# Kernel optimization log

Hardware: AMD Instinct MI355X
Metric: run time of the kernel (lower is better)

Reference implementation:

```python
import jax, jax.numpy as jnp
import numpy as np

K = 3       # kernel_size
STRIDE = 1
PAD = 1


def conv2d(x, w, b):
    y = jax.lax.conv_general_dilated(
        x, w, window_strides=(STRIDE, STRIDE), padding=[(PAD, PAD), (PAD, PAD)],
        dimension_numbers=('NCHW', 'OIHW', 'NCHW'))
    return y + b[None, :, None, None]


def setup_inputs() -> dict:
    key = jax.random.key(0)
    ks = jax.random.split(key, 4)
    B, Cin, Cout, H, W = 8, 64, 64, 64, 64
    kk = K * K
    x = jax.random.normal(ks[0], (B, Cin, H, W), jnp.float32)
    # offset / modulator convs (zero-init in the original; use small random weights
    # so offsets are nontrivial but realistic sub-pixel scale)
    w_off = jax.random.normal(ks[1], (2 * kk, Cin, K, K), jnp.float32) * 0.01
    b_off = jnp.zeros((2 * kk,), jnp.float32)
    w_mod = jax.random.normal(ks[2], (kk, Cin, K, K), jnp.float32) * 0.01
    b_mod = jnp.zeros((kk,), jnp.float32)
    # main deformable conv weight, Kaiming-ish scale
    w = jax.random.normal(ks[3], (Cout, Cin, K, K), jnp.float32) * (1.0 / np.sqrt(Cin * kk))
    b = jnp.zeros((Cout,), jnp.float32)
    return {"x": x, "w_off": w_off, "b_off": b_off,
            "w_mod": w_mod, "b_mod": b_mod, "w": w, "b": b}


def deform_conv2d(x, offset, mask, w, b):
    # torchvision deform_conv2d semantics, deformable_groups=1, groups=1.
    B, C, H, W = x.shape
    kk = K * K
    Ho = (H + 2 * PAD - K) // STRIDE + 1
    Wo = (W + 2 * PAD - K) // STRIDE + 1
    # offset channels are interleaved (dy, dx) pairs per kernel tap
    off = offset.reshape(B, kk, 2, Ho, Wo)
    kh, kw = jnp.meshgrid(jnp.arange(K), jnp.arange(K), indexing='ij')
    kh = kh.reshape(kk).astype(x.dtype)
    kw = kw.reshape(kk).astype(x.dtype)
    base_y = (jnp.arange(Ho) * STRIDE - PAD).astype(x.dtype)
    base_x = (jnp.arange(Wo) * STRIDE - PAD).astype(x.dtype)
    # sampling coordinates in input space: [B, kk, Ho, Wo]
    ys = base_y[None, None, :, None] + kh[None, :, None, None] + off[:, :, 0]
    xs = base_x[None, None, None, :] + kw[None, :, None, None] + off[:, :, 1]
    y0 = jnp.floor(ys)
    x0 = jnp.floor(xs)

    def gather(yi, xi):
        yc = jnp.clip(yi, 0, H - 1).astype(jnp.int32)
        xc = jnp.clip(xi, 0, W - 1).astype(jnp.int32)
        # per-batch fancy gather: [C, H, W] indexed by [kk, Ho, Wo] -> [C, kk, Ho, Wo]
        return jax.vmap(lambda img, yb, xb: img[:, yb, xb])(x, yc, xc)

    acc = jnp.zeros((B, C, kk, Ho, Wo), x.dtype)
    for dy, dx in ((0, 0), (0, 1), (1, 0), (1, 1)):
        yi = y0 + dy
        xi = x0 + dx
        wgt = (1.0 - jnp.abs(ys - yi)) * (1.0 - jnp.abs(xs - xi))
        # zero-padding semantics: corners outside the input contribute 0
        valid = (yi >= 0) & (yi <= H - 1) & (xi >= 0) & (xi <= W - 1)
        wgt = jnp.where(valid, wgt, 0.0)
        acc = acc + gather(yi, xi) * wgt[:, None]
    # modulate with sigmoid mask [B, kk, Ho, Wo], then contract with conv weight
    sampled = acc * mask[:, None]
    out = jnp.einsum('bcfij,ocf->boij', sampled, w.reshape(w.shape[0], C, kk))
    return out + b[None, :, None, None]


def reference(x, w_off, b_off, w_mod, b_mod, w, b):
    offset = conv2d(x, w_off, b_off)
    mask = jax.nn.sigmoid(conv2d(x, w_mod, b_mod))
    return deform_conv2d(x, offset, mask, w, b)
```

## Files before the change

### kernel.cpp

```cpp
#include <hip/hip_runtime.h>
#include <math.h>

#define HW    64
#define NPIX  32768

typedef __attribute__((ext_vector_type(8))) short bf16x8;
typedef __attribute__((ext_vector_type(8))) short short8v;
typedef __attribute__((ext_vector_type(4))) float f32x4;

static __device__ inline short f2bf(float f) {
    union { float f; unsigned u; } v; v.f = f;
    unsigned r = v.u + 0x7fff + ((v.u >> 16) & 1);
    return (short)(r >> 16);
}
static __device__ inline float bf2f(short s) {
    union { unsigned u; float f; } v; v.u = ((unsigned)(unsigned short)s) << 16;
    return v.f;
}

__global__ void k_prep(const float* __restrict__ w,
                       const float* __restrict__ w_off,
                       const float* __restrict__ w_mod,
                       short* __restrict__ wt2, short* __restrict__ wc2) {
    int t = blockIdx.x * 256 + threadIdx.x;
    if (t < 9 * 64 * 64) {
        int c = t & 63, o = (t >> 6) & 63, f = t >> 12;
        wt2[t] = f2bf(w[(o * 64 + c) * 9 + f]);
    }
    int u = t - 9 * 64 * 64;
    if (u >= 0 && u < 9 * 32 * 64) {
        int c = u & 63, ch = (u >> 6) & 31, f = u >> 11;
        float v = 0.f;
        if (ch < 18)      v = w_off[(ch * 64 + c) * 9 + f];
        else if (ch < 27) v = w_mod[((ch - 18) * 64 + c) * 9 + f];
        wc2[u] = f2bf(v);
    }
}

__global__ __launch_bounds__(256) void k_transpose(const float* __restrict__ x,
                                                   short* __restrict__ xt) {
    __shared__ float s[64 * 65];
    int tid = threadIdx.x;
    int by  = blockIdx.x;
    int b = by >> 6, y = by & 63;
    const float* xb = x + ((size_t)b * 64) * 4096 + y * 64;
    #pragma unroll
    for (int q = 0; q < 4; ++q) {
        int fi = q * 256 + tid;
        int c = fi >> 4, xq = (fi & 15) * 4;
        float4 v = *(const float4*)(xb + (size_t)c * 4096 + xq);
        s[c * 65 + xq + 0] = v.x; s[c * 65 + xq + 1] = v.y;
        s[c * 65 + xq + 2] = v.z; s[c * 65 + xq + 3] = v.w;
    }
    __syncthreads();
    short* dst = xt + ((size_t)(b * 64 + y)) * 4096;
    #pragma unroll
    for (int q = 0; q < 4; ++q) {
        int fi = q * 256 + tid;
        int xx = fi >> 4, c = (fi & 15) * 4;
        short4 v = make_short4(f2bf(s[(c + 0) * 65 + xx]), f2bf(s[(c + 1) * 65 + xx]),
                               f2bf(s[(c + 2) * 65 + xx]), f2bf(s[(c + 3) * 65 + xx]));
        *(short4*)(dst + xx * 64 + c) = v;
    }
}

__global__ __launch_bounds__(128, 2) void k_fused(
        const short* __restrict__ xt,
        const short* __restrict__ wc2, const short* __restrict__ wt2,
        const float* __restrict__ b_off, const float* __restrict__ b_mod,
        const float* __restrict__ bias, float* __restrict__ out) {
    __shared__ __align__(16) char smem[19328];
    short*  s_in  = (short*)smem;
    float4* s_mW  = (float4*)smem;
    int4*   s_mO  = (int4*)(smem + 4608);
    float*  s_fin = (float*)smem;
    float*  s_out = (float*)(smem + 14720);

    int tid  = threadIdx.x;
    int lane = tid & 63;
    int wv   = __builtin_amdgcn_readfirstlane((int)(tid >> 6));
    int blk  = blockIdx.x;
    int b = blk >> 7, i = (blk >> 1) & 63, jb = (blk & 1) * 32;
    const short* xb = xt + (size_t)b * 262144;

    int arow = lane & 15;
    int cg   = lane >> 4;
    int cgb  = cg * 8;

    for (int u = tid; u < 816; u += 128) {
        int r = u / 272, rem = u - r * 272;
        int slot = rem >> 3, c8 = (rem & 7) << 3;
        int y = i - 1 + r, gx = jb + slot - 1;
        short8v v = (short8v){0,0,0,0,0,0,0,0};
        if (((unsigned)y < 64u) & ((unsigned)gx < 64u))
            v = *(const short8v*)(xb + ((y << 6) + gx) * 64 + c8);
        *(short8v*)(s_in + (r * 34 + slot) * 72 + c8) = v;
    }
    __syncthreads();

    f32x4 accc[2];
    accc[0] = (f32x4){0.f,0.f,0.f,0.f};
    accc[1] = (f32x4){0.f,0.f,0.f,0.f};
    #pragma unroll
    for (int ky = 0; ky < 3; ++ky)
        #pragma unroll
        for (int kx = 0; kx < 3; ++kx) {
            int f = ky * 3 + kx;
            bf16x8 bq[2];
            #pragma unroll
            for (int kk = 0; kk < 2; ++kk)
                bq[kk] = *(const bf16x8*)(wc2 + (f * 32 + wv * 16 + arow) * 64 + kk * 32 + cgb);
            #pragma unroll
            for (int kk = 0; kk < 2; ++kk)
                #pragma unroll
                for (int mm = 0; mm < 2; ++mm) {
                    const short* ap = s_in + (ky * 34 + mm * 16 + arow + kx) * 72 + kk * 32 + cgb;
                    accc[mm] = __builtin_amdgcn_mfma_f32_16x16x32_bf16(
                        *(const bf16x8*)ap, bq[kk], accc[mm], 0, 0, 0);
                }
        }
    {
        int ch = wv * 16 + arow;
        #pragma unroll
        for (int mm = 0; mm < 2; ++mm)
            #pragma unroll
            for (int r = 0; r < 4; ++r)
                s_out[ch * 36 + mm * 16 + cg * 4 + r] = accc[mm][r];
    }
    __syncthreads();

    for (int u = tid; u < 288; u += 128) {
        int f = u >> 5, p = u & 31;
        float dy = s_out[(2 * f)     * 36 + p] + b_off[2 * f];
        float dx = s_out[(2 * f + 1) * 36 + p] + b_off[2 * f + 1];
        float mv = s_out[(18 + f)    * 36 + p] + b_mod[f];
        float m  = 1.f / (1.f + expf(-mv));

        float ys  = (float)(i - 1 + f / 3) + dy;
        float xs2 = (float)(jb + p - 1 + f % 3) + dx;
        float y0f = floorf(ys), x0f = floorf(xs2);
        int   y0  = (int)y0f,   x0  = (int)x0f;
        float fy = ys - y0f, fx = xs2 - x0f;

        bool vy0 = (unsigned)y0       < 64u, vy1 = (unsigned)(y0 + 1) < 64u;
        bool vx0 = (unsigned)x0       < 64u, vx1 = (unsigned)(x0 + 1) < 64u;
        float w00 = (vy0 & vx0) ? (1.f - fy) * (1.f - fx) * m : 0.f;
        float w01 = (vy0 & vx1) ? (1.f - fy) * fx         * m : 0.f;
        float w10 = (vy1 & vx0) ? fy         * (1.f - fx) * m : 0.f;
        float w11 = (vy1 & vx1) ? fy         * fx         * m : 0.f;

        int y0c = min(max(y0, 0), 63), y1c = min(max(y0 + 1, 0), 63);
        int x0c = min(max(x0, 0), 63), x1c = min(max(x0 + 1, 0), 63);

        s_mW[u] = make_float4(w00, w01, w10, w11);
        s_mO[u] = make_int4((y0c * 64 + x0c) * 64, (y0c * 64 + x1c) * 64,
                            (y1c * 64 + x0c) * 64, (y1c * 64 + x1c) * 64);
    }
    __syncthreads();

    f32x4 acc[4];
    #pragma unroll
    for (int mf = 0; mf < 4; ++mf) acc[mf] = (f32x4){0.f,0.f,0.f,0.f};

    #pragma unroll
    for (int f = 0; f < 9; ++f) {
        int mi = f * 32 + wv * 16 + arow;
        float4 mW = s_mW[mi];
        int4   mO = s_mO[mi];
        bf16x8 c0[2], c1[2], c2[2], c3[2];
        #pragma unroll
        for (int kk = 0; kk < 2; ++kk) {
            int base = kk * 32 + cgb;
            c0[kk] = *(const bf16x8*)(xb + mO.x + base);
            c1[kk] = *(const bf16x8*)(xb + mO.y + base);
            c2[kk] = *(const bf16x8*)(xb + mO.z + base);
            c3[kk] = *(const bf16x8*)(xb + mO.w + base);
        }
        bf16x8 sf[2];
        #pragma unroll
        for (int kk = 0; kk < 2; ++kk)
            #pragma unroll
            for (int j = 0; j < 8; ++j) {
                float s = mW.x * bf2f(c0[kk][j]) + mW.y * bf2f(c1[kk][j])
                        + mW.z * bf2f(c2[kk][j]) + mW.w * bf2f(c3[kk][j]);
                sf[kk][j] = f2bf(s);
            }
        #pragma unroll
        for (int kk = 0; kk < 2; ++kk)
            #pragma unroll
            for (int mf = 0; mf < 4; ++mf) {
                const short* wp = wt2 + (f * 64 + mf * 16 + arow) * 64 + kk * 32 + cgb;
                acc[mf] = __builtin_amdgcn_mfma_f32_16x16x32_bf16(
                    *(const bf16x8*)wp, sf[kk], acc[mf], 0, 0, 0);
            }
    }
    __syncthreads();

    #pragma unroll
    for (int mf = 0; mf < 4; ++mf)
        #pragma unroll
        for (int r = 0; r < 4; ++r)
            s_fin[(mf * 16 + cg * 4 + r) * 33 + wv * 16 + arow] = acc[mf][r];
    __syncthreads();
    {
        int o  = tid >> 1;
        int ph = (tid & 1) * 16;
        float bv = bias[o];
        float* op = out + (((size_t)(b * 64 + o)) * 64 + i) * 64 + jb + ph;
        #pragma unroll
        for (int q = 0; q < 4; ++q) {
            float4 v;
            v.x = s_fin[o * 33 + ph + q * 4 + 0] + bv;
            v.y = s_fin[o * 33 + ph + q * 4 + 1] + bv;
            v.z = s_fin[o * 33 + ph + q * 4 + 2] + bv;
            v.w = s_fin[o * 33 + ph + q * 4 + 3] + bv;
            *(float4*)(op + q * 4) = v;
        }
    }
}

extern "C" void kernel_launch(void* const* d_in, const int* in_sizes, int n_in,
                              void* d_out, int out_size, void* d_ws, size_t ws_size,
                              hipStream_t stream) {
    const float* x     = (const float*)d_in[0];
    const float* w_off = (const float*)d_in[1];
    const float* b_off = (const float*)d_in[2];
    const float* w_mod = (const float*)d_in[3];
    const float* b_mod = (const float*)d_in[4];
    const float* w     = (const float*)d_in[5];
    const float* bias  = (const float*)d_in[6];
    float* out = (float*)d_out;

    char* ws = (char*)d_ws;
    short* xt  = (short*)(ws);
    short* wt2 = (short*)(ws + 4194304);
    short* wc2 = (short*)(ws + 4268032);

    hipLaunchKernelGGL(k_prep,      dim3(216),  dim3(256), 0, stream, w, w_off, w_mod, wt2, wc2);
    hipLaunchKernelGGL(k_transpose, dim3(512),  dim3(256), 0, stream, x, xt);
    hipLaunchKernelGGL(k_fused,     dim3(1024), dim3(128), 0, stream,
                       xt, wc2, wt2, b_off, b_mod, bias, out);
}
```

Measured before the change: 57.42 us.

## Stage 5x36 input halo in swizzled LDS and gather bilinear corners from it

The fused kernel now loads a wider 5-row by 36-column input halo into XOR-swizzled shared memory. Bilinear corner samples that fall inside this window are read from LDS, and only out-of-window corners go to global memory. Blocks grow to 256 threads: the offset conv is split across four waves, and the deformable GEMM is split over the channel dimension, with a two-way reduction through shared memory at the end. This trades more LDS use and an extra reduction for fewer scattered global gathers and more waves per block.

New measurement: 49.57 us. 1.16x faster.

```diff
diff --git a/kernel.cpp b/kernel.cpp
--- a/kernel.cpp
+++ b/kernel.cpp
@@ -64,17 +64,16 @@
     }
 }
 
-__global__ __launch_bounds__(128, 2) void k_fused(
+__global__ __launch_bounds__(256, 4) void k_fused(
         const short* __restrict__ xt,
         const short* __restrict__ wc2, const short* __restrict__ wt2,
         const float* __restrict__ b_off, const float* __restrict__ b_mod,
         const float* __restrict__ bias, float* __restrict__ out) {
-    __shared__ __align__(16) char smem[19328];
-    short*  s_in  = (short*)smem;
-    float4* s_mW  = (float4*)smem;
-    int4*   s_mO  = (int4*)(smem + 4608);
-    float*  s_fin = (float*)smem;
-    float*  s_out = (float*)(smem + 14720);
+    __shared__ __align__(16) char smem[39936];
+    float*  s_out = (float*)(smem + 23040);
+    float4* s_mW  = (float4*)(smem + 27648);
+    int4*   s_mO  = (int4*)(smem + 32256);
+    float*  s_red = (float*)(smem + 23040);
 
     int tid  = threadIdx.x;
     int lane = tid & 63;
@@ -87,49 +86,44 @@
     int cg   = lane >> 4;
     int cgb  = cg * 8;
 
-    for (int u = tid; u < 816; u += 128) {
-        int r = u / 272, rem = u - r * 272;
-        int slot = rem >> 3, c8 = (rem & 7) << 3;
-        int y = i - 1 + r, gx = jb + slot - 1;
+    for (int u = tid; u < 1440; u += 256) {
+        int cell = u >> 3, chunk = u & 7;
+        int r = cell / 36, cc = cell - r * 36;
+        int y = i - 2 + r, gx = jb - 2 + cc;
         short8v v = (short8v){0,0,0,0,0,0,0,0};
         if (((unsigned)y < 64u) & ((unsigned)gx < 64u))
-            v = *(const short8v*)(xb + ((y << 6) + gx) * 64 + c8);
-        *(short8v*)(s_in + (r * 34 + slot) * 72 + c8) = v;
-    }
-    __syncthreads();
-
-    f32x4 accc[2];
-    accc[0] = (f32x4){0.f,0.f,0.f,0.f};
-    accc[1] = (f32x4){0.f,0.f,0.f,0.f};
-    #pragma unroll
-    for (int ky = 0; ky < 3; ++ky)
-        #pragma unroll
-        for (int kx = 0; kx < 3; ++kx) {
-            int f = ky * 3 + kx;
-            bf16x8 bq[2];
+            v = *(const short8v*)(xb + ((y << 6) + gx) * 64 + chunk * 8);
+        *(short8v*)(smem + cell * 128 + ((chunk * 16) ^ ((cell & 7) << 4))) = v;
+    }
+    __syncthreads();
+
+    {
+        int mh = wv & 1, nh = wv >> 1;
+        f32x4 accc = (f32x4){0.f, 0.f, 0.f, 0.f};
+        #pragma unroll
+        for (int ky = 0; ky < 3; ++ky)
             #pragma unroll
-            for (int kk = 0; kk < 2; ++kk)
-                bq[kk] = *(const bf16x8*)(wc2 + (f * 32 + wv * 16 + arow) * 64 + kk * 32 + cgb);
-            #pragma unroll
-            for (int kk = 0; kk < 2; ++kk)
+            for (int kx = 0; kx < 3; ++kx) {
+                int f = ky * 3 + kx;
                 #pragma unroll
-                for (int mm = 0; mm < 2; ++mm) {
-                    const short* ap = s_in + (ky * 34 + mm * 16 + arow + kx) * 72 + kk * 32 + cgb;
-                    accc[mm] = __builtin_amdgcn_mfma_f32_16x16x32_bf16(
-                        *(const bf16x8*)ap, bq[kk], accc[mm], 0, 0, 0);
+                for (int kk = 0; kk < 2; ++kk) {
+                    bf16x8 bq = *(const bf16x8*)(wc2 + (f * 32 + nh * 16 + arow) * 64
+                                                 + kk * 32 + cgb);
+                    int cell = (ky + 1) * 36 + mh * 16 + arow + kx + 1;
+                    const char* ap = smem + cell * 128
+                                   + ((kk * 64 + cg * 16) ^ ((cell & 7) << 4));
+                    accc = __builtin_amdgcn_mfma_f32_16x16x32_bf16(
+                        *(const bf16x8*)ap, bq, accc, 0, 0, 0);
                 }
-        }
-    {
-        int ch = wv * 16 + arow;
-        #pragma unroll
-        for (int mm = 0; mm < 2; ++mm)
-            #pragma unroll
-            for (int r = 0; r < 4; ++r)
-                s_out[ch * 36 + mm * 16 + cg * 4 + r] = accc[mm][r];
-    }
-    __syncthreads();
-
-    for (int u = tid; u < 288; u += 128) {
+            }
+        __syncthreads();
+        #pragma unroll
+        for (int r = 0; r < 4; ++r)
+            s_out[(nh * 16 + arow) * 36 + mh * 16 + cg * 4 + r] = accc[r];
+    }
+    __syncthreads();
+
+    for (int u = tid; u < 288; u += 256) {
         int f = u >> 5, p = u & 31;
         float dy = s_out[(2 * f)     * 36 + p] + b_off[2 * f];
         float dx = s_out[(2 * f + 1) * 36 + p] + b_off[2 * f + 1];
@@ -152,47 +146,56 @@
         int y0c = min(max(y0, 0), 63), y1c = min(max(y0 + 1, 0), 63);
         int x0c = min(max(x0, 0), 63), x1c = min(max(x0 + 1, 0), 63);
 
+        #define ENCODE(yc, xc) ({                                          \
+            int wr_ = (yc) - (i - 2), wc_ = (xc) - (jb - 2);               \
+            bool inw_ = ((unsigned)wr_ < 5u) & ((unsigned)wc_ < 36u);      \
+            int cell_ = wr_ * 36 + wc_;                                    \
+            inw_ ? cell_ * 128                                             \
+                 : (int)((((yc) * 64 + (xc)) * 128) | 0x80000000); })
+
         s_mW[u] = make_float4(w00, w01, w10, w11);
-        s_mO[u] = make_int4((y0c * 64 + x0c) * 64, (y0c * 64 + x1c) * 64,
-                            (y1c * 64 + x0c) * 64, (y1c * 64 + x1c) * 64);
-    }
-    __syncthreads();
-
+        s_mO[u] = make_int4(ENCODE(y0c, x0c), ENCODE(y0c, x1c),
+                            ENCODE(y1c, x0c), ENCODE(y1c, x1c));
+        #undef ENCODE
+    }
+    __syncthreads();
+
+    int ph  = wv & 1;
+    int kk2 = wv >> 1;
+    int kbyte = kk2 * 64 + cg * 16;
     f32x4 acc[4];
     #pragma unroll
-    for (int mf = 0; mf < 4; ++mf) acc[mf] = (f32x4){0.f,0.f,0.f,0.f};
+    for (int mf = 0; mf < 4; ++mf) acc[mf] = (f32x4){0.f, 0.f, 0.f, 0.f};
 
     #pragma unroll
     for (int f = 0; f < 9; ++f) {
-        int mi = f * 32 + wv * 16 + arow;
+        int mi = f * 32 + ph * 16 + arow;
         float4 mW = s_mW[mi];
         int4   mO = s_mO[mi];
-        bf16x8 c0[2], c1[2], c2[2], c3[2];
-        #pragma unroll
-        for (int kk = 0; kk < 2; ++kk) {
-            int base = kk * 32 + cgb;
-            c0[kk] = *(const bf16x8*)(xb + mO.x + base);
-            c1[kk] = *(const bf16x8*)(xb + mO.y + base);
-            c2[kk] = *(const bf16x8*)(xb + mO.z + base);
-            c3[kk] = *(const bf16x8*)(xb + mO.w + base);
-        }
-        bf16x8 sf[2];
-        #pragma unroll
-        for (int kk = 0; kk < 2; ++kk)
-            #pragma unroll
-            for (int j = 0; j < 8; ++j) {
-                float s = mW.x * bf2f(c0[kk][j]) + mW.y * bf2f(c1[kk][j])
-                        + mW.z * bf2f(c2[kk][j]) + mW.w * bf2f(c3[kk][j]);
-                sf[kk][j] = f2bf(s);
-            }
-        #pragma unroll
-        for (int kk = 0; kk < 2; ++kk)
-            #pragma unroll
-            for (int mf = 0; mf < 4; ++mf) {
-                const short* wp = wt2 + (f * 64 + mf * 16 + arow) * 64 + kk * 32 + cgb;
-                acc[mf] = __builtin_amdgcn_mfma_f32_16x16x32_bf16(
-                    *(const bf16x8*)wp, sf[kk], acc[mf], 0, 0, 0);
-            }
+        bf16x8 c[4];
+        int enc0 = mO.x, enc1 = mO.y, enc2 = mO.z, enc3 = mO.w;
+        #define CORNER(idx, enc) {                                              \
+            int cb = (enc) >= 0 ? (enc) : 0;                                    \
+            c[idx] = *(const bf16x8*)(smem + cb + (kbyte ^ (((cb >> 7) & 7) << 4))); \
+            if ((enc) < 0)                                                      \
+                c[idx] = *(const bf16x8*)((const char*)xb                       \
+                         + ((enc) & 0x7fffffff) + kbyte);                       \
+        }
+        CORNER(0, enc0) CORNER(1, enc1) CORNER(2, enc2) CORNER(3, enc3)
+        #undef CORNER
+        bf16x8 sf;
+        #pragma unroll
+        for (int j = 0; j < 8; ++j) {
+            float s = mW.x * bf2f(c[0][j]) + mW.y * bf2f(c[1][j])
+                    + mW.z * bf2f(c[2][j]) + mW.w * bf2f(c[3][j]);
+            sf[j] = f2bf(s);
+        }
+        #pragma unroll
+        for (int mf = 0; mf < 4; ++mf) {
+            const short* wp = wt2 + (f * 64 + mf * 16 + arow) * 64 + kk2 * 32 + cgb;
+            acc[mf] = __builtin_amdgcn_mfma_f32_16x16x32_bf16(
+                *(const bf16x8*)wp, sf, acc[mf], 0, 0, 0);
+        }
     }
     __syncthreads();
 
@@ -200,20 +203,20 @@
     for (int mf = 0; mf < 4; ++mf)
         #pragma unroll
         for (int r = 0; r < 4; ++r)
-            s_fin[(mf * 16 + cg * 4 + r) * 33 + wv * 16 + arow] = acc[mf][r];
+            s_red[kk2 * 2112 + (mf * 16 + cg * 4 + r) * 33 + ph * 16 + arow] = acc[mf][r];
     __syncthreads();
     {
-        int o  = tid >> 1;
-        int ph = (tid & 1) * 16;
+        int o  = tid >> 2;
+        int pg = (tid & 3) * 8;
         float bv = bias[o];
-        float* op = out + (((size_t)(b * 64 + o)) * 64 + i) * 64 + jb + ph;
-        #pragma unroll
-        for (int q = 0; q < 4; ++q) {
+        float* op = out + (((size_t)(b * 64 + o)) * 64 + i) * 64 + jb + pg;
+        #pragma unroll
+        for (int q = 0; q < 2; ++q) {
             float4 v;
-            v.x = s_fin[o * 33 + ph + q * 4 + 0] + bv;
-            v.y = s_fin[o * 33 + ph + q * 4 + 1] + bv;
-            v.z = s_fin[o * 33 + ph + q * 4 + 2] + bv;
-            v.w = s_fin[o * 33 + ph + q * 4 + 3] + bv;
+            v.x = s_red[o * 33 + pg + q * 4 + 0] + s_red[2112 + o * 33 + pg + q * 4 + 0] + bv;
+            v.y = s_red[o * 33 + pg + q * 4 + 1] + s_red[2112 + o * 33 + pg + q * 4 + 1] + bv;
+            v.z = s_red[o * 33 + pg + q * 4 + 2] + s_red[2112 + o * 33 + pg + q * 4 + 2] + bv;
+            v.w = s_red[o * 33 + pg + q * 4 + 3] + s_red[2112 + o * 33 + pg + q * 4 + 3] + bv;
             *(float4*)(op + q * 4) = v;
         }
     }
@@ -238,6 +241,6 @@
 
     hipLaunchKernelGGL(k_prep,      dim3(216),  dim3(256), 0, stream, w, w_off, w_mod, wt2, wc2);
     hipLaunchKernelGGL(k_transpose, dim3(512),  dim3(256), 0, stream, x, xt);
-    hipLaunchKernelGGL(k_fused,     dim3(1024), dim3(128), 0, stream,
+    hipLaunchKernelGGL(k_fused,     dim3(1024), dim3(256), 0, stream,
                        xt, wc2, wt2, b_off, b_mod, bias, out);
 }
```

## Split fused deform conv into offset-meta, bias-init, and per-tap gather kernels with atomics

Applied to the files above, without the earlier changes.

Breaks the single fused kernel into three kernels. The first computes the offset/mask conv for full rows and writes the bilinear weights and offsets to global workspace, using an XOR-swizzled LDS layout. The second initialises the output with the bias. The third launches one 64-thread block per 16 pixels and kernel tap, gathers and MFMAs, then accumulates into the output with float atomics. The aim is more parallelism and shorter per-block dependency chains, at the cost of extra global metadata traffic, two more launches, and 9-way atomic contention on the output.

New measurement: 97.71 us. 70.2% more time.

```diff
diff --git a/kernel.cpp b/kernel.cpp
--- a/kernel.cpp
+++ b/kernel.cpp
@@ -64,80 +64,75 @@
     }
 }
 
-__global__ __launch_bounds__(128, 2) void k_fused(
-        const short* __restrict__ xt,
-        const short* __restrict__ wc2, const short* __restrict__ wt2,
+__global__ __launch_bounds__(256) void k_convmeta(
+        const short* __restrict__ xt, const short* __restrict__ wc2,
         const float* __restrict__ b_off, const float* __restrict__ b_mod,
-        const float* __restrict__ bias, float* __restrict__ out) {
-    __shared__ __align__(16) char smem[19328];
-    short*  s_in  = (short*)smem;
-    float4* s_mW  = (float4*)smem;
-    int4*   s_mO  = (int4*)(smem + 4608);
-    float*  s_fin = (float*)smem;
-    float*  s_out = (float*)(smem + 14720);
+        float4* __restrict__ metaW, int4* __restrict__ metaO) {
+    __shared__ __align__(16) char smem[34816];
+    float* s_out = (float*)(smem + 26112);
 
     int tid  = threadIdx.x;
     int lane = tid & 63;
     int wv   = __builtin_amdgcn_readfirstlane((int)(tid >> 6));
     int blk  = blockIdx.x;
-    int b = blk >> 7, i = (blk >> 1) & 63, jb = (blk & 1) * 32;
-    const short* xb = xt + (size_t)b * 262144;
-
-    int arow = lane & 15;
-    int cg   = lane >> 4;
-    int cgb  = cg * 8;
-
-    for (int u = tid; u < 816; u += 128) {
-        int r = u / 272, rem = u - r * 272;
-        int slot = rem >> 3, c8 = (rem & 7) << 3;
-        int y = i - 1 + r, gx = jb + slot - 1;
+    int b = blk >> 6, i = blk & 63;
+    const short* xs = xt + (size_t)b * 262144;
+
+    int arow = lane & 15, cg = lane >> 4, cgb = cg * 8;
+
+    for (int u = tid; u < 1632; u += 256) {
+        int cell = u >> 3, chunk = u & 7;
+        int r = cell / 68, cc = cell - r * 68;
+        int y = i - 1 + r, gx = cc - 2;
         short8v v = (short8v){0,0,0,0,0,0,0,0};
         if (((unsigned)y < 64u) & ((unsigned)gx < 64u))
-            v = *(const short8v*)(xb + ((y << 6) + gx) * 64 + c8);
-        *(short8v*)(s_in + (r * 34 + slot) * 72 + c8) = v;
+            v = *(const short8v*)(xs + ((y << 6) + gx) * 64 + chunk * 8);
+        *(short8v*)(smem + cell * 128 + ((chunk * 16) ^ ((cell & 7) << 4))) = v;
     }
     __syncthreads();
 
-    f32x4 accc[2];
-    accc[0] = (f32x4){0.f,0.f,0.f,0.f};
-    accc[1] = (f32x4){0.f,0.f,0.f,0.f};
-    #pragma unroll
-    for (int ky = 0; ky < 3; ++ky)
-        #pragma unroll
-        for (int kx = 0; kx < 3; ++kx) {
-            int f = ky * 3 + kx;
-            bf16x8 bq[2];
+    {
+        int nf = wv & 1, mg = wv >> 1;
+        f32x4 accc[2];
+        accc[0] = (f32x4){0.f,0.f,0.f,0.f};
+        accc[1] = (f32x4){0.f,0.f,0.f,0.f};
+        #pragma unroll
+        for (int ky = 0; ky < 3; ++ky)
             #pragma unroll
-            for (int kk = 0; kk < 2; ++kk)
-                bq[kk] = *(const bf16x8*)(wc2 + (f * 32 + wv * 16 + arow) * 64 + kk * 32 + cgb);
-            #pragma unroll
-            for (int kk = 0; kk < 2; ++kk)
+            for (int kx = 0; kx < 3; ++kx) {
+                int f = ky * 3 + kx;
                 #pragma unroll
-                for (int mm = 0; mm < 2; ++mm) {
-                    const short* ap = s_in + (ky * 34 + mm * 16 + arow + kx) * 72 + kk * 32 + cgb;
-                    accc[mm] = __builtin_amdgcn_mfma_f32_16x16x32_bf16(
-                        *(const bf16x8*)ap, bq[kk], accc[mm], 0, 0, 0);
+                for (int kk = 0; kk < 2; ++kk) {
+                    bf16x8 bq = *(const bf16x8*)(wc2 + (f * 32 + nf * 16 + arow) * 64
+                                                 + kk * 32 + cgb);
+                    #pragma unroll
+                    for (int mm = 0; mm < 2; ++mm) {
+                        int cell = ky * 68 + mg * 32 + mm * 16 + arow + kx + 1;
+                        const char* ap = smem + cell * 128
+                                       + ((kk * 64 + cg * 16) ^ ((cell & 7) << 4));
+                        accc[mm] = __builtin_amdgcn_mfma_f32_16x16x32_bf16(
+                            *(const bf16x8*)ap, bq, accc[mm], 0, 0, 0);
+                    }
                 }
-        }
-    {
-        int ch = wv * 16 + arow;
+            }
         #pragma unroll
         for (int mm = 0; mm < 2; ++mm)
             #pragma unroll
             for (int r = 0; r < 4; ++r)
-                s_out[ch * 36 + mm * 16 + cg * 4 + r] = accc[mm][r];
+                s_out[(nf * 16 + arow) * 66 + mg * 32 + mm * 16 + cg * 4 + r] = accc[mm][r];
     }
     __syncthreads();
 
-    for (int u = tid; u < 288; u += 128) {
-        int f = u >> 5, p = u & 31;
-        float dy = s_out[(2 * f)     * 36 + p] + b_off[2 * f];
-        float dx = s_out[(2 * f + 1) * 36 + p] + b_off[2 * f + 1];
-        float mv = s_out[(18 + f)    * 36 + p] + b_mod[f];
+    int pixBase = blk * 64;
+    for (int u = tid; u < 576; u += 256) {
+        int f = u >> 6, p = u & 63;
+        float dy = s_out[(2 * f)     * 66 + p] + b_off[2 * f];
+        float dx = s_out[(2 * f + 1) * 66 + p] + b_off[2 * f + 1];
+        float mv = s_out[(18 + f)    * 66 + p] + b_mod[f];
         float m  = 1.f / (1.f + expf(-mv));
 
         float ys  = (float)(i - 1 + f / 3) + dy;
-        float xs2 = (float)(jb + p - 1 + f % 3) + dx;
+        float xs2 = (float)(p - 1 + f % 3) + dx;
         float y0f = floorf(ys), x0f = floorf(xs2);
         int   y0  = (int)y0f,   x0  = (int)x0f;
         float fy = ys - y0f, fx = xs2 - x0f;
@@ -152,71 +147,72 @@
         int y0c = min(max(y0, 0), 63), y1c = min(max(y0 + 1, 0), 63);
         int x0c = min(max(x0, 0), 63), x1c = min(max(x0 + 1, 0), 63);
 
-        s_mW[u] = make_float4(w00, w01, w10, w11);
-        s_mO[u] = make_int4((y0c * 64 + x0c) * 64, (y0c * 64 + x1c) * 64,
-                            (y1c * 64 + x0c) * 64, (y1c * 64 + x1c) * 64);
-    }
-    __syncthreads();
+        metaW[f * NPIX + pixBase + p] = make_float4(w00, w01, w10, w11);
+        metaO[f * NPIX + pixBase + p] = make_int4(((y0c << 6) + x0c) * 128,
+                                                  ((y0c << 6) + x1c) * 128,
+                                                  ((y1c << 6) + x0c) * 128,
+                                                  ((y1c << 6) + x1c) * 128);
+    }
+}
+
+__global__ __launch_bounds__(256) void k_zero(const float* __restrict__ bias,
+                                              float* __restrict__ out) {
+    int t = blockIdx.x * 256 + threadIdx.x;
+    int base = t * 4;
+    float bv = bias[(base >> 12) & 63];
+    *(float4*)(out + base) = make_float4(bv, bv, bv, bv);
+}
+
+__global__ __launch_bounds__(64) void k_gather(
+        const short* __restrict__ xt,
+        const float4* __restrict__ metaW, const int4* __restrict__ metaO,
+        const short* __restrict__ wt2, float* __restrict__ out) {
+    int lane = threadIdx.x;
+    int f    = blockIdx.y;
+    int pixBase = blockIdx.x * 16;
+    int arow = lane & 15, cg = lane >> 4, cgb = cg * 8;
+    int P = pixBase + arow;
+    int b = P >> 12;
+    const char* xbb = (const char*)(xt + (size_t)b * 262144);
+
+    float4 mW = metaW[f * NPIX + P];
+    int4   mO = metaO[f * NPIX + P];
 
     f32x4 acc[4];
     #pragma unroll
     for (int mf = 0; mf < 4; ++mf) acc[mf] = (f32x4){0.f,0.f,0.f,0.f};
 
     #pragma unroll
-    for (int f = 0; f < 9; ++f) {
-        int mi = f * 32 + wv * 16 + arow;
-        float4 mW = s_mW[mi];
-        int4   mO = s_mO[mi];
-        bf16x8 c0[2], c1[2], c2[2], c3[2];
-        #pragma unroll
-        for (int kk = 0; kk < 2; ++kk) {
-            int base = kk * 32 + cgb;
-            c0[kk] = *(const bf16x8*)(xb + mO.x + base);
-            c1[kk] = *(const bf16x8*)(xb + mO.y + base);
-            c2[kk] = *(const bf16x8*)(xb + mO.z + base);
-            c3[kk] = *(const bf16x8*)(xb + mO.w + base);
+    for (int kk = 0; kk < 2; ++kk) {
+        int off = kk * 64 + cg * 16;
+        bf16x8 c0 = *(const bf16x8*)(xbb + mO.x + off);
+        bf16x8 c1 = *(const bf16x8*)(xbb + mO.y + off);
+        bf16x8 c2 = *(const bf16x8*)(xbb + mO.z + off);
+        bf16x8 c3 = *(const bf16x8*)(xbb + mO.w + off);
+        bf16x8 sf;
+        #pragma unroll
+        for (int j = 0; j < 8; ++j) {
+            float s = mW.x * bf2f(c0[j]) + mW.y * bf2f(c1[j])
+                    + mW.z * bf2f(c2[j]) + mW.w * bf2f(c3[j]);
+            sf[j] = f2bf(s);
         }
-        bf16x8 sf[2];
-        #pragma unroll
-        for (int kk = 0; kk < 2; ++kk)
-            #pragma unroll
-            for (int j = 0; j < 8; ++j) {
-                float s = mW.x * bf2f(c0[kk][j]) + mW.y * bf2f(c1[kk][j])
-                        + mW.z * bf2f(c2[kk][j]) + mW.w * bf2f(c3[kk][j]);
-                sf[kk][j] = f2bf(s);
-            }
-        #pragma unroll
-        for (int kk = 0; kk < 2; ++kk)
-            #pragma unroll
-            for (int mf = 0; mf < 4; ++mf) {
-                const short* wp = wt2 + (f * 64 + mf * 16 + arow) * 64 + kk * 32 + cgb;
-                acc[mf] = __builtin_amdgcn_mfma_f32_16x16x32_bf16(
-                    *(const bf16x8*)wp, sf[kk], acc[mf], 0, 0, 0);
-            }
-    }
-    __syncthreads();
-
+        #pragma unroll
+        for (int mf = 0; mf < 4; ++mf) {
+            const short* wp = wt2 + (f * 64 + mf * 16 + arow) * 64 + kk * 32 + cgb;
+            acc[mf] = __builtin_amdgcn_mfma_f32_16x16x32_bf16(
+                *(const bf16x8*)wp, sf, acc[mf], 0, 0, 0);
+        }
+    }
+
+    int ii = (P >> 6) & 63, jj = P & 63;
+    float* ob = out + (size_t)b * 262144 + ii * 64 + jj;
     #pragma unroll
     for (int mf = 0; mf < 4; ++mf)
         #pragma unroll
-        for (int r = 0; r < 4; ++r)
-            s_fin[(mf * 16 + cg * 4 + r) * 33 + wv * 16 + arow] = acc[mf][r];
-    __syncthreads();
-    {
-        int o  = tid >> 1;
-        int ph = (tid & 1) * 16;
-        float bv = bias[o];
-        float* op = out + (((size_t)(b * 64 + o)) * 64 + i) * 64 + jb + ph;
-        #pragma unroll
-        for (int q = 0; q < 4; ++q) {
-            float4 v;
-            v.x = s_fin[o * 33 + ph + q * 4 + 0] + bv;
-            v.y = s_fin[o * 33 + ph + q * 4 + 1] + bv;
-            v.z = s_fin[o * 33 + ph + q * 4 + 2] + bv;
-            v.w = s_fin[o * 33 + ph + q * 4 + 3] + bv;
-            *(float4*)(op + q * 4) = v;
+        for (int r = 0; r < 4; ++r) {
+            int o = mf * 16 + cg * 4 + r;
+            atomicAdd(ob + (size_t)o * 4096, acc[mf][r]);
         }
-    }
 }
 
 extern "C" void kernel_launch(void* const* d_in, const int* in_sizes, int n_in,
@@ -232,12 +228,17 @@
     float* out = (float*)d_out;
 
     char* ws = (char*)d_ws;
-    short* xt  = (short*)(ws);
-    short* wt2 = (short*)(ws + 4194304);
-    short* wc2 = (short*)(ws + 4268032);
-
-    hipLaunchKernelGGL(k_prep,      dim3(216),  dim3(256), 0, stream, w, w_off, w_mod, wt2, wc2);
-    hipLaunchKernelGGL(k_transpose, dim3(512),  dim3(256), 0, stream, x, xt);
-    hipLaunchKernelGGL(k_fused,     dim3(1024), dim3(128), 0, stream,
-                       xt, wc2, wt2, b_off, b_mod, bias, out);
-}
+    short*  xt    = (short*)(ws);
+    short*  wt2   = (short*)(ws + 4194304);
+    short*  wc2   = (short*)(ws + 4268032);
+    float4* metaW = (float4*)(ws + 4304896);
+    int4*   metaO = (int4*)(ws + 9023488);
+
+    hipLaunchKernelGGL(k_prep,      dim3(216),       dim3(256), 0, stream, w, w_off, w_mod, wt2, wc2);
+    hipLaunchKernelGGL(k_transpose, dim3(512),       dim3(256), 0, stream, x, xt);
+    hipLaunchKernelGGL(k_convmeta,  dim3(512),       dim3(256), 0, stream,
+                       xt, wc2, b_off, b_mod, metaW, metaO);
+    hipLaunchKernelGGL(k_zero,      dim3(2048),      dim3(256), 0, stream, bias, out);
+    hipLaunchKernelGGL(k_gather,    dim3(2048, 9),   dim3(64),  0, stream,
+                       xt, metaW, metaO, wt2, out);
+}
```
